# Kernel optimization log

Measured on AMD Instinct MI355X. Metric: run time of the kernel, lower is better.

## Reference

```python
import jax, jax.numpy as jnp
import numpy as np

D_MODEL = 1024
N_HEADS = 16
HEAD_DIM = D_MODEL // N_HEADS


def setup_inputs() -> dict:
    key = jax.random.key(0)
    ks = jax.random.split(key, 5)
    q = jax.random.normal(ks[0], (2, 2048, D_MODEL), dtype=jnp.float32)
    Wq = jax.random.normal(ks[1], (D_MODEL, D_MODEL), dtype=jnp.float32) * (1.0 / np.sqrt(D_MODEL))
    bq = jax.random.normal(ks[2], (D_MODEL,), dtype=jnp.float32) * 0.01
    Wo = jax.random.normal(ks[3], (D_MODEL, D_MODEL), dtype=jnp.float32) * (1.0 / np.sqrt(D_MODEL))
    bo = jax.random.normal(ks[4], (D_MODEL,), dtype=jnp.float32) * 0.01
    return {"q": q, "Wq": Wq, "bq": bq, "Wo": Wo, "bo": bo}


def reference(q, Wq, bq, Wo, bo):
    bs, S, dim = q.shape
    # NOTE: original module (bug-faithfully) projects Q, K and V all with WQ.
    proj = q @ Wq.T + bq  # [B, S, D]
    h = proj.reshape(bs, S, N_HEADS, HEAD_DIM).transpose(0, 2, 1, 3)  # [B, H, S, Dh]
    qh, kh, vh = h, h, h
    scale = HEAD_DIM ** -0.5
    attn = jnp.einsum('bhqd,bhkd->bhqk', qh, kh) * scale  # [B, H, S, S]
    scores = jax.nn.softmax(attn, axis=-1)
    # dropout is identity in inference mode
    vals = jnp.einsum('bhqk,bhkd->bhqd', scores, vh)  # [B, H, S, Dh]
    vals = vals.transpose(0, 2, 1, 3).reshape(bs, S, dim)
    return vals @ Wo.T + bo
```

## Files before the change

### kernel.cpp

```cpp
#include <hip/hip_runtime.h>

#define D_MODEL 1024
#define N_HEADS 16
#define HEAD_DIM 64
#define SEQ 2048
#define BATCH 2
#define M_TOTAL (BATCH*SEQ)

typedef __bf16 bf16;
typedef __bf16 bf16x8 __attribute__((ext_vector_type(8)));
typedef __bf16 bf16x4 __attribute__((ext_vector_type(4)));
typedef float  floatx4 __attribute__((ext_vector_type(4)));
typedef short  shortx4 __attribute__((ext_vector_type(4)));

#if __has_builtin(__builtin_amdgcn_exp2f)
#define EXP2F(x) __builtin_amdgcn_exp2f(x)
#else
#define EXP2F(x) __expf(0.69314718f * (x))
#endif

__device__ __forceinline__ floatx4 mfma16(bf16x4 a, bf16x4 b, floatx4 c) {
#if __has_builtin(__builtin_amdgcn_mfma_f32_16x16x16_bf16)
    return __builtin_amdgcn_mfma_f32_16x16x16_bf16(a, b, c, 0, 0, 0);
#else
    return __builtin_amdgcn_mfma_f32_16x16x16bf16_1k(
        __builtin_bit_cast(shortx4, a), __builtin_bit_cast(shortx4, b), c, 0, 0, 0);
#endif
}

__device__ __forceinline__ void gl2lds16(const bf16* g, bf16* l) {
    __builtin_amdgcn_global_load_lds(
        (const __attribute__((address_space(1))) unsigned int*)g,
        (__attribute__((address_space(3))) unsigned int*)l, 16, 0, 0);
}

__global__ void cvt_all(const float* __restrict__ q, const float* __restrict__ Wq,
                        const float* __restrict__ Wo, bf16* __restrict__ qb,
                        bf16* __restrict__ wqb, bf16* __restrict__ wob) {
    int i = blockIdx.x * 256 + threadIdx.x;
    const float* src; bf16* dst; int off;
    if (i < 1048576)      { src = q;  dst = qb;  off = i; }
    else if (i < 1310720) { src = Wq; dst = wqb; off = i - 1048576; }
    else                  { src = Wo; dst = wob; off = i - 1310720; }
    float4 v = ((const float4*)src)[off];
    bf16x4 o;
    o[0] = (bf16)v.x; o[1] = (bf16)v.y; o[2] = (bf16)v.z; o[3] = (bf16)v.w;
    ((bf16x4*)dst)[off] = o;
}

template<int MODE>
__global__ __launch_bounds__(256)
void gemm_bt_bias_t(const bf16* __restrict__ A, const bf16* __restrict__ B,
                    const float* __restrict__ bias, void* __restrict__ Cout,
                    bf16* __restrict__ Cout2, int M, int N, int K)
{
    __shared__ __align__(16) bf16 smem[24576];
    bf16* As = smem;
    bf16* Bs = smem + 16384;

    const int tid  = threadIdx.x;
    const int lane = tid & 63;
    const int wave = tid >> 6;
    const int quad = lane >> 4;
    const int l16  = lane & 15;
    const int lin  = blockIdx.x;
    const int m0   = ((lin & 7) * 4 + ((lin >> 3) & 3)) * 128;
    const int n0   = (lin >> 5) * 64;
    const int wm   = (wave >> 1) * 64;
    const int wn   = (wave & 1) * 32;

    floatx4 acc[4][2];
#pragma unroll
    for (int i = 0; i < 4; i++)
#pragma unroll
        for (int j = 0; j < 2; j++) acc[i][j] = (floatx4){0.f, 0.f, 0.f, 0.f};

    auto issue = [&](int buf, int k0) {
#pragma unroll
        for (int it = 0; it < 4; it++) {
            int s = it * 256 + tid;
            int row = s >> 3, cl = (s & 7) ^ (row & 7);
            gl2lds16(A + (size_t)(m0 + row) * K + k0 + cl * 8, &As[buf * 8192 + s * 8]);
        }
#pragma unroll
        for (int it = 0; it < 2; it++) {
            int s = it * 256 + tid;
            int row = s >> 3, cl = (s & 7) ^ (row & 7);
            gl2lds16(B + (size_t)(n0 + row) * K + k0 + cl * 8, &Bs[buf * 4096 + s * 8]);
        }
    };
    issue(0, 0);
    int buf = 0;
    for (int k0 = 0; k0 < K; k0 += 64, buf ^= 1) {
        __syncthreads();
        if (k0 + 64 < K) issue(buf ^ 1, k0 + 64);
#pragma unroll
        for (int ks = 0; ks < 2; ks++) {
            bf16x8 af[4], bfr[2];
#pragma unroll
            for (int i = 0; i < 4; i++) {
                int row = wm + i * 16 + l16;
                int phys = (ks * 4 + quad) ^ (row & 7);
                af[i] = *(const bf16x8*)&As[buf * 8192 + row * 64 + phys * 8];
            }
#pragma unroll
            for (int j = 0; j < 2; j++) {
                int row = wn + j * 16 + l16;
                int phys = (ks * 4 + quad) ^ (row & 7);
                bfr[j] = *(const bf16x8*)&Bs[buf * 4096 + row * 64 + phys * 8];
            }
#pragma unroll
            for (int i = 0; i < 4; i++)
#pragma unroll
                for (int j = 0; j < 2; j++)
                    acc[i][j] = __builtin_amdgcn_mfma_f32_16x16x32_bf16(
                        af[i], bfr[j], acc[i][j], 0, 0, 0);
        }
    }

    if constexpr (MODE == 0) {
        float* C = (float*)Cout;
#pragma unroll
        for (int j = 0; j < 2; j++) {
            int col  = n0 + wn + j * 16 + l16;
            float bv = bias[col];
#pragma unroll
            for (int i = 0; i < 4; i++) {
                int rbase = m0 + wm + i * 16 + quad * 4;
#pragma unroll
                for (int r = 0; r < 4; r++)
                    C[(size_t)(rbase + r) * N + col] = acc[i][j][r] + bv;
            }
        }
    } else {
        bf16* Cb = (bf16*)Cout;
        const int h  = n0 >> 6;
        const int b  = m0 >> 11;
        bf16x4 tile[4][2];
#pragma unroll
        for (int j = 0; j < 2; j++) {
            int dL   = wn + j * 16 + l16;
            float bv = bias[n0 + dL];
#pragma unroll
            for (int i = 0; i < 4; i++) {
                int sl = wm + i * 16 + quad * 4;
                int s0 = (m0 & 2047) + sl;
#pragma unroll
                for (int r = 0; r < 4; r++) {
                    float v = acc[i][j][r] + bv;
                    tile[i][j][r] = (bf16)v;
                    Cb[(((size_t)(b * N_HEADS + h) * SEQ + (s0 + r)) << 6) + dL] = (bf16)v;
                }
            }
        }
        __syncthreads();
#pragma unroll
        for (int j = 0; j < 2; j++) {
            int dL = wn + j * 16 + l16;
#pragma unroll
            for (int i = 0; i < 4; i++) {
                int sl = wm + i * 16 + quad * 4;
                *(bf16x4*)&smem[dL * 128 + (((sl >> 3) ^ (dL & 15)) * 8) + (sl & 7)] =
                    tile[i][j];
            }
        }
        __syncthreads();
        {
            int dL    = tid >> 2;
            int sbase = m0 & 2047;
            bf16* dstrow = Cout2 + ((size_t)(b * N_HEADS + h) * 64 + dL) * SEQ + sbase;
#pragma unroll
            for (int cc = 0; cc < 4; cc++) {
                int c    = (tid & 3) * 4 + cc;
                int phys = c ^ (dL & 15);
                *(bf16x8*)(dstrow + c * 8) = *(const bf16x8*)&smem[dL * 128 + phys * 8];
            }
        }
    }
}

__global__ __launch_bounds__(256, 4)
void flash_attn(const bf16* __restrict__ projbf, const bf16* __restrict__ projT,
                float* __restrict__ Opart, float* __restrict__ Lpart)
{
    __shared__ __align__(16) bf16 Ks[2][64 * 64];
    __shared__ __align__(16) bf16 Vt[2][64 * 64];

    const int tid  = threadIdx.x;
    const int lane = tid & 63;
    const int wave = tid >> 6;
    const int quad = lane >> 4;
    const int l16  = lane & 15;
    const int lin  = blockIdx.x;
    const int bh   = (lin & 7) * 4 + (lin >> 8);
    const int q0   = ((lin >> 4) & 15) * 128;
    const int ksp  = (lin >> 3) & 1;
    const int kbase = ksp * 1024;
    const bf16* hK  = projbf + (size_t)bh * SEQ * 64;
    const bf16* hVt = projT  + (size_t)bh * 64 * SEQ;
    const int wq0  = wave * 32;

    bf16x8 qf[2][2];
#pragma unroll
    for (int nbi = 0; nbi < 2; nbi++)
#pragma unroll
        for (int ks = 0; ks < 2; ks++)
            qf[nbi][ks] = *(const bf16x8*)(hK + (size_t)(q0 + wq0 + nbi * 16 + l16) * 64
                                           + ks * 32 + quad * 8);

    floatx4 oacc[4][2];
#pragma unroll
    for (int mb = 0; mb < 4; mb++)
#pragma unroll
        for (int nbi = 0; nbi < 2; nbi++) oacc[mb][nbi] = (floatx4){0.f, 0.f, 0.f, 0.f};
    float lsum[2] = {0.f, 0.f};

    auto issue = [&](int buf, int k0) {
#pragma unroll
        for (int it = 0; it < 2; it++) {
            int s = it * 256 + tid;
            int row = s >> 3, cl = (s & 7) ^ (row & 7);
            gl2lds16(hK + (size_t)(k0 + row) * 64 + cl * 8, &Ks[buf][s * 8]);
        }
#pragma unroll
        for (int it = 0; it < 2; it++) {
            int s = it * 256 + tid;
            int row = s >> 3, cl = (s & 7) ^ (row & 7);
            gl2lds16(hVt + (size_t)row * SEQ + k0 + cl * 8, &Vt[buf][s * 8]);
        }
    };
    issue(0, kbase);
    int buf = 0;
    for (int k0 = kbase; k0 < kbase + 1024; k0 += 64, buf ^= 1) {
        __syncthreads();
        if (k0 + 64 < kbase + 1024) issue(buf ^ 1, k0 + 64);

#pragma unroll
        for (int kc = 0; kc < 4; kc++) {
            int krow = kc * 16 + l16;
            bf16x8 kf0 = *(const bf16x8*)&Ks[buf][krow * 64 + ((quad ^ (krow & 7)) * 8)];
            bf16x8 kf1 = *(const bf16x8*)&Ks[buf][krow * 64 + (((4 + quad) ^ (krow & 7)) * 8)];
            bf16x4 p4[2];
#pragma unroll
            for (int nbi = 0; nbi < 2; nbi++) {
                floatx4 s = __builtin_amdgcn_mfma_f32_16x16x32_bf16(
                    kf0, qf[nbi][0], (floatx4){0.f, 0.f, 0.f, 0.f}, 0, 0, 0);
                s = __builtin_amdgcn_mfma_f32_16x16x32_bf16(
                    kf1, qf[nbi][1], s, 0, 0, 0);
                float ps = 0.f;
#pragma unroll
                for (int r = 0; r < 4; r++) {
                    float p = EXP2F(fmaf(s[r], 0.18033688f, -23.083120f));
                    p4[nbi][r] = (bf16)p; ps += p;
                }
                lsum[nbi] += ps;
            }
#pragma unroll
            for (int mb = 0; mb < 4; mb++) {
                int vrow = mb * 16 + l16;
                int c    = kc * 2 + (quad >> 1);
                bf16x4 vf = *(const bf16x4*)&Vt[buf][vrow * 64
                                + ((c ^ (vrow & 7)) * 8) + (quad & 1) * 4];
#pragma unroll
                for (int nbi = 0; nbi < 2; nbi++)
                    oacc[mb][nbi] = mfma16(vf, p4[nbi], oacc[mb][nbi]);
            }
        }
    }

#pragma unroll
    for (int nbi = 0; nbi < 2; nbi++) {
        lsum[nbi] += __shfl_xor(lsum[nbi], 16);
        lsum[nbi] += __shfl_xor(lsum[nbi], 32);
    }
#pragma unroll
    for (int nbi = 0; nbi < 2; nbi++) {
        int qh = bh * SEQ + q0 + wq0 + nbi * 16 + l16;
        float* orow = Opart + ((size_t)ksp * 65536 + qh) * 64;
#pragma unroll
        for (int mb = 0; mb < 4; mb++)
            *(floatx4*)&orow[mb * 16 + quad * 4] = oacc[mb][nbi];
    }
    if (quad < 2) {
        int qh = bh * SEQ + q0 + wq0 + quad * 16 + l16;
        Lpart[ksp * 65536 + qh] = lsum[quad];
    }
}

__global__ __launch_bounds__(256)
void combine_o(const float* __restrict__ Opart, const float* __restrict__ Lpart,
               bf16* __restrict__ vals)
{
    const int lin = blockIdx.x;
    const int qh  = ((lin & 7) * 128 + (lin >> 3)) * 64 + (threadIdx.x >> 2);
    const int dq  = (threadIdx.x & 3) * 16;
    const float* p0 = Opart + (size_t)qh * 64 + dq;
    const float* p1 = p0 + (size_t)65536 * 64;
    const float rinv = 1.0f / (Lpart[qh] + Lpart[65536 + qh]);
    const int bh = qh >> 11, b = bh >> 4, h = bh & 15, q = qh & 2047;
    bf16* dst = vals + ((size_t)b * SEQ + q) * D_MODEL + h * 64 + dq;
#pragma unroll
    for (int w = 0; w < 2; w++) {
        bf16x8 o;
#pragma unroll
        for (int i = 0; i < 2; i++) {
            float4 a  = ((const float4*)p0)[w * 2 + i];
            float4 bb = ((const float4*)p1)[w * 2 + i];
            o[i * 4 + 0] = (bf16)((a.x + bb.x) * rinv);
            o[i * 4 + 1] = (bf16)((a.y + bb.y) * rinv);
            o[i * 4 + 2] = (bf16)((a.z + bb.z) * rinv);
            o[i * 4 + 3] = (bf16)((a.w + bb.w) * rinv);
        }
        *(bf16x8*)(dst + w * 8) = o;
    }
}

extern "C" void kernel_launch(void* const* d_in, const int* in_sizes, int n_in,
                              void* d_out, int out_size, void* d_ws, size_t ws_size,
                              hipStream_t stream)
{
    const float* q  = (const float*)d_in[0];
    const float* Wq = (const float*)d_in[1];
    const float* bq = (const float*)d_in[2];
    const float* Wo = (const float*)d_in[3];
    const float* bo = (const float*)d_in[4];
    float* out = (float*)d_out;

    char* ws = (char*)d_ws;
    bf16*  qbf    = (bf16*)(ws);
    bf16*  Wqbf   = (bf16*)(ws + (size_t)( 8 << 20));
    bf16*  Wobf   = (bf16*)(ws + (size_t)(10 << 20));
    bf16*  projbf = (bf16*)(ws + (size_t)(12 << 20));
    bf16*  projT  = (bf16*)(ws + (size_t)(20 << 20));
    bf16*  valsb  = (bf16*)(ws + (size_t)(28 << 20));
    float* Opart  = (float*)(ws + (size_t)(36 << 20));
    float* Lpart  = (float*)(ws + (size_t)(68 << 20));

    cvt_all<<<6144, 256, 0, stream>>>(q, Wq, Wo, qbf, Wqbf, Wobf);

    gemm_bt_bias_t<1><<<512, 256, 0, stream>>>(qbf, Wqbf, bq, (void*)projbf,
                                               projT, M_TOTAL, D_MODEL, D_MODEL);

    flash_attn<<<1024, 256, 0, stream>>>(projbf, projT, Opart, Lpart);
    combine_o<<<1024, 256, 0, stream>>>(Opart, Lpart, valsb);

    gemm_bt_bias_t<0><<<512, 256, 0, stream>>>(valsb, Wobf, bo, (void*)out,
                                               nullptr, M_TOTAL, D_MODEL, D_MODEL);
}
```

Measured before the change: 167.8 us.

## Triple-buffer GEMM and attention loads, drop split-K combine kernel

```diff
diff --git a/kernel.cpp b/kernel.cpp
--- a/kernel.cpp
+++ b/kernel.cpp
@@ -33,6 +33,8 @@
         (const __attribute__((address_space(1))) unsigned int*)g,
         (__attribute__((address_space(3))) unsigned int*)l, 16, 0, 0);
 }
+
+#define WAITBAR(N) asm volatile("s_waitcnt vmcnt(" #N ")\n\ts_barrier" ::: "memory")
 
 __global__ void cvt_all(const float* __restrict__ q, const float* __restrict__ Wq,
                         const float* __restrict__ Wo, bf16* __restrict__ qb,
@@ -49,14 +51,12 @@
 }
 
 template<int MODE>
-__global__ __launch_bounds__(256)
+__global__ __launch_bounds__(256, 2)
 void gemm_bt_bias_t(const bf16* __restrict__ A, const bf16* __restrict__ B,
                     const float* __restrict__ bias, void* __restrict__ Cout,
                     bf16* __restrict__ Cout2, int M, int N, int K)
 {
-    __shared__ __align__(16) bf16 smem[24576];
-    bf16* As = smem;
-    bf16* Bs = smem + 16384;
+    __shared__ __align__(16) bf16 smem[36864];
 
     const int tid  = threadIdx.x;
     const int lane = tid & 63;
@@ -75,25 +75,22 @@
 #pragma unroll
         for (int j = 0; j < 2; j++) acc[i][j] = (floatx4){0.f, 0.f, 0.f, 0.f};
 
-    auto issue = [&](int buf, int k0) {
+    auto issue = [&](int base, int k0) {
 #pragma unroll
         for (int it = 0; it < 4; it++) {
             int s = it * 256 + tid;
             int row = s >> 3, cl = (s & 7) ^ (row & 7);
-            gl2lds16(A + (size_t)(m0 + row) * K + k0 + cl * 8, &As[buf * 8192 + s * 8]);
+            gl2lds16(A + (size_t)(m0 + row) * K + k0 + cl * 8, &smem[base + s * 8]);
         }
 #pragma unroll
         for (int it = 0; it < 2; it++) {
             int s = it * 256 + tid;
             int row = s >> 3, cl = (s & 7) ^ (row & 7);
-            gl2lds16(B + (size_t)(n0 + row) * K + k0 + cl * 8, &Bs[buf * 4096 + s * 8]);
+            gl2lds16(B + (size_t)(n0 + row) * K + k0 + cl * 8, &smem[base + 8192 + s * 8]);
         }
     };
-    issue(0, 0);
-    int buf = 0;
-    for (int k0 = 0; k0 < K; k0 += 64, buf ^= 1) {
-        __syncthreads();
-        if (k0 + 64 < K) issue(buf ^ 1, k0 + 64);
+
+    auto compute = [&](int base) {
 #pragma unroll
         for (int ks = 0; ks < 2; ks++) {
             bf16x8 af[4], bfr[2];
@@ -101,13 +98,13 @@
             for (int i = 0; i < 4; i++) {
                 int row = wm + i * 16 + l16;
                 int phys = (ks * 4 + quad) ^ (row & 7);
-                af[i] = *(const bf16x8*)&As[buf * 8192 + row * 64 + phys * 8];
+                af[i] = *(const bf16x8*)&smem[base + row * 64 + phys * 8];
             }
 #pragma unroll
             for (int j = 0; j < 2; j++) {
                 int row = wn + j * 16 + l16;
                 int phys = (ks * 4 + quad) ^ (row & 7);
-                bfr[j] = *(const bf16x8*)&Bs[buf * 4096 + row * 64 + phys * 8];
+                bfr[j] = *(const bf16x8*)&smem[base + 8192 + row * 64 + phys * 8];
             }
 #pragma unroll
             for (int i = 0; i < 4; i++)
@@ -116,7 +113,18 @@
                     acc[i][j] = __builtin_amdgcn_mfma_f32_16x16x32_bf16(
                         af[i], bfr[j], acc[i][j], 0, 0, 0);
         }
-    }
+    };
+
+    const int NT = K >> 6;
+    issue(0, 0);
+    issue(12288, 64);
+    for (int t = 0; t < NT - 1; ++t) {
+        WAITBAR(6);
+        if (t + 2 < NT) issue(((t + 2) % 3) * 12288, (t + 2) << 6);
+        compute((t % 3) * 12288);
+    }
+    WAITBAR(0);
+    compute(((NT - 1) % 3) * 12288);
 
     if constexpr (MODE == 0) {
         float* C = (float*)Cout;
@@ -179,12 +187,12 @@
     }
 }
 
-__global__ __launch_bounds__(256, 4)
+__global__ __launch_bounds__(256, 3)
 void flash_attn(const bf16* __restrict__ projbf, const bf16* __restrict__ projT,
-                float* __restrict__ Opart, float* __restrict__ Lpart)
+                bf16* __restrict__ vals)
 {
-    __shared__ __align__(16) bf16 Ks[2][64 * 64];
-    __shared__ __align__(16) bf16 Vt[2][64 * 64];
+    __shared__ __align__(16) bf16 Ks[3][64 * 64];
+    __shared__ __align__(16) bf16 Vt[3][64 * 64];
 
     const int tid  = threadIdx.x;
     const int lane = tid & 63;
@@ -192,10 +200,8 @@
     const int quad = lane >> 4;
     const int l16  = lane & 15;
     const int lin  = blockIdx.x;
-    const int bh   = (lin & 7) * 4 + (lin >> 8);
-    const int q0   = ((lin >> 4) & 15) * 128;
-    const int ksp  = (lin >> 3) & 1;
-    const int kbase = ksp * 1024;
+    const int bh   = (lin & 7) * 4 + (lin >> 7);
+    const int q0   = ((lin >> 3) & 15) * 128;
     const bf16* hK  = projbf + (size_t)bh * SEQ * 64;
     const bf16* hVt = projT  + (size_t)bh * 64 * SEQ;
     const int wq0  = wave * 32;
@@ -207,6 +213,7 @@
         for (int ks = 0; ks < 2; ks++)
             qf[nbi][ks] = *(const bf16x8*)(hK + (size_t)(q0 + wq0 + nbi * 16 + l16) * 64
                                            + ks * 32 + quad * 8);
+    asm volatile("s_waitcnt vmcnt(0)" ::: "memory");
 
     floatx4 oacc[4][2];
 #pragma unroll
@@ -229,12 +236,8 @@
             gl2lds16(hVt + (size_t)row * SEQ + k0 + cl * 8, &Vt[buf][s * 8]);
         }
     };
-    issue(0, kbase);
-    int buf = 0;
-    for (int k0 = kbase; k0 < kbase + 1024; k0 += 64, buf ^= 1) {
-        __syncthreads();
-        if (k0 + 64 < kbase + 1024) issue(buf ^ 1, k0 + 64);
-
+
+    auto compute = [&](int buf) {
 #pragma unroll
         for (int kc = 0; kc < 4; kc++) {
             int krow = kc * 16 + l16;
@@ -266,52 +269,35 @@
                     oacc[mb][nbi] = mfma16(vf, p4[nbi], oacc[mb][nbi]);
             }
         }
-    }
+    };
+
+    issue(0, 0);
+    issue(1, 64);
+    for (int t = 0; t < 31; ++t) {
+        WAITBAR(4);
+        if (t < 30) issue((t + 2) % 3, (t + 2) * 64);
+        compute(t % 3);
+    }
+    WAITBAR(0);
+    compute(1);
 
 #pragma unroll
     for (int nbi = 0; nbi < 2; nbi++) {
         lsum[nbi] += __shfl_xor(lsum[nbi], 16);
         lsum[nbi] += __shfl_xor(lsum[nbi], 32);
     }
+    const int b = bh >> 4, h = bh & 15;
 #pragma unroll
     for (int nbi = 0; nbi < 2; nbi++) {
-        int qh = bh * SEQ + q0 + wq0 + nbi * 16 + l16;
-        float* orow = Opart + ((size_t)ksp * 65536 + qh) * 64;
-#pragma unroll
-        for (int mb = 0; mb < 4; mb++)
-            *(floatx4*)&orow[mb * 16 + quad * 4] = oacc[mb][nbi];
-    }
-    if (quad < 2) {
-        int qh = bh * SEQ + q0 + wq0 + quad * 16 + l16;
-        Lpart[ksp * 65536 + qh] = lsum[quad];
-    }
-}
-
-__global__ __launch_bounds__(256)
-void combine_o(const float* __restrict__ Opart, const float* __restrict__ Lpart,
-               bf16* __restrict__ vals)
-{
-    const int lin = blockIdx.x;
-    const int qh  = ((lin & 7) * 128 + (lin >> 3)) * 64 + (threadIdx.x >> 2);
-    const int dq  = (threadIdx.x & 3) * 16;
-    const float* p0 = Opart + (size_t)qh * 64 + dq;
-    const float* p1 = p0 + (size_t)65536 * 64;
-    const float rinv = 1.0f / (Lpart[qh] + Lpart[65536 + qh]);
-    const int bh = qh >> 11, b = bh >> 4, h = bh & 15, q = qh & 2047;
-    bf16* dst = vals + ((size_t)b * SEQ + q) * D_MODEL + h * 64 + dq;
-#pragma unroll
-    for (int w = 0; w < 2; w++) {
-        bf16x8 o;
-#pragma unroll
-        for (int i = 0; i < 2; i++) {
-            float4 a  = ((const float4*)p0)[w * 2 + i];
-            float4 bb = ((const float4*)p1)[w * 2 + i];
-            o[i * 4 + 0] = (bf16)((a.x + bb.x) * rinv);
-            o[i * 4 + 1] = (bf16)((a.y + bb.y) * rinv);
-            o[i * 4 + 2] = (bf16)((a.z + bb.z) * rinv);
-            o[i * 4 + 3] = (bf16)((a.w + bb.w) * rinv);
-        }
-        *(bf16x8*)(dst + w * 8) = o;
+        float rinv = 1.0f / lsum[nbi];
+        int q = q0 + wq0 + nbi * 16 + l16;
+#pragma unroll
+        for (int mb = 0; mb < 4; mb++) {
+            bf16x4 o4;
+#pragma unroll
+            for (int r = 0; r < 4; r++) o4[r] = (bf16)(oacc[mb][nbi][r] * rinv);
+            *(bf16x4*)&vals[((size_t)b * SEQ + q) * D_MODEL + h * 64 + mb * 16 + quad * 4] = o4;
+        }
     }
 }
 
@@ -327,22 +313,19 @@
     float* out = (float*)d_out;
 
     char* ws = (char*)d_ws;
-    bf16*  qbf    = (bf16*)(ws);
-    bf16*  Wqbf   = (bf16*)(ws + (size_t)( 8 << 20));
-    bf16*  Wobf   = (bf16*)(ws + (size_t)(10 << 20));
-    bf16*  projbf = (bf16*)(ws + (size_t)(12 << 20));
-    bf16*  projT  = (bf16*)(ws + (size_t)(20 << 20));
-    bf16*  valsb  = (bf16*)(ws + (size_t)(28 << 20));
-    float* Opart  = (float*)(ws + (size_t)(36 << 20));
-    float* Lpart  = (float*)(ws + (size_t)(68 << 20));
+    bf16* qbf    = (bf16*)(ws);
+    bf16* Wqbf   = (bf16*)(ws + (size_t)( 8 << 20));
+    bf16* Wobf   = (bf16*)(ws + (size_t)(10 << 20));
+    bf16* projbf = (bf16*)(ws + (size_t)(12 << 20));
+    bf16* projT  = (bf16*)(ws + (size_t)(20 << 20));
+    bf16* valsb  = (bf16*)(ws + (size_t)(28 << 20));
 
     cvt_all<<<6144, 256, 0, stream>>>(q, Wq, Wo, qbf, Wqbf, Wobf);
 
     gemm_bt_bias_t<1><<<512, 256, 0, stream>>>(qbf, Wqbf, bq, (void*)projbf,
                                                projT, M_TOTAL, D_MODEL, D_MODEL);
 
-    flash_attn<<<1024, 256, 0, stream>>>(projbf, projT, Opart, Lpart);
-    combine_o<<<1024, 256, 0, stream>>>(Opart, Lpart, valsb);
+    flash_attn<<<512, 256, 0, stream>>>(projbf, projT, valsb);
 
     gemm_bt_bias_t<0><<<512, 256, 0, stream>>>(valsb, Wobf, bo, (void*)out,
                                                nullptr, M_TOTAL, D_MODEL, D_MODEL);
```

Measured after the change: 153.8 us. 8.3% less time.
